# Kernel tuning notes

Measured on AMD Instinct MI355X. Metric: run time of the kernel, lower is better.

## Reference

```python
import jax, jax.numpy as jnp
import numpy as np

TEMPERATURE = 1.0  # anneal_state_params['tempature'] at init
EPS_ZERO = 1e-5
EPS_DIV = 1e-29

N, M, K, D = 200000, 64, 16, 32

def setup_inputs() -> dict:
    key = jax.random.key(0)
    k1, k2, k3 = jax.random.split(key, 3)
    T = jax.random.normal(k1, (N, D), dtype=jnp.float32)
    alpha = jax.random.uniform(k2, (M, K, D), dtype=jnp.float32)  # np.random.rand init
    th = jnp.zeros((M, K), dtype=jnp.float32)
    # ambiguity thresholds: column 0 = pos (>0), column 1 = neg (<0)
    a = jax.random.uniform(k3, (M, K, 2), dtype=jnp.float32) * 0.5 + 0.1
    amb = a * jnp.array([1.0, -1.0], dtype=jnp.float32)
    return {"T": T, "alpha": alpha, "th": th, "amb": amb}

def reference(T, alpha, th, amb):
    # per-fern softmax over the feature axis of alpha*temperature
    sa = jax.nn.softmax(alpha * TEMPERATURE, axis=-1)          # (M, K, D)
    # batched fern projections: one einsum replaces the per-fern matmul loop
    temp = jnp.einsum('nd,mkd->nmk', T, sa)                    # (N, M, K)
    temp = jnp.where(jnp.abs(temp) < EPS_ZERO, 0.0, temp)
    b = temp - th[None, :, :]                                  # subtract threshold
    pos = amb[None, :, :, 0]                                   # (1, M, K)
    neg = amb[None, :, :, 1]
    B = jnp.clip((b - neg) / (pos - neg + EPS_DIV), 0.0, 1.0)  # (N, M, K)
    return B
```

## Files before the change

kernel.cpp:

```cpp
#include <hip/hip_runtime.h>
#include <math.h>

#define N_TOT 200000
#define D_    32
#define MK    1024
#define EPS_ZERO 1e-5f
#define EPS_DIV  1e-29f

#define BN   64
#define BMK  256
#define NB_N (N_TOT / BN)
#define NB_MK (MK / BMK)

typedef __attribute__((ext_vector_type(8))) short short8;
typedef __attribute__((ext_vector_type(4))) float f32x4;

__device__ __forceinline__ unsigned short f2bf(float x) {
    unsigned int u = __float_as_uint(x);
    u += 0x7FFFu + ((u >> 16) & 1u);
    return (unsigned short)(u >> 16);
}
__device__ __forceinline__ float bf2f(unsigned short h) {
    return __uint_as_float(((unsigned int)h) << 16);
}

__global__ __launch_bounds__(256) void prep_kernel(
    const float* __restrict__ alpha, const float* __restrict__ th,
    const float* __restrict__ amb,
    unsigned short* __restrict__ Whi, unsigned short* __restrict__ Wlo,
    float* __restrict__ ot)
{
    int mk = blockIdx.x * 256 + threadIdx.x;
    if (mk >= MK) return;
    float v[D_];
    float mx = -1e30f;
#pragma unroll
    for (int d = 0; d < D_; ++d) { v[d] = alpha[mk * D_ + d]; mx = fmaxf(mx, v[d]); }
    float sum = 0.f;
#pragma unroll
    for (int d = 0; d < D_; ++d) { v[d] = expf(v[d] - mx); sum += v[d]; }
    float pos = amb[mk * 2 + 0];
    float neg = amb[mk * 2 + 1];
    float s  = 1.0f / (pos - neg + EPS_DIV);
    float si = s / sum;
#pragma unroll
    for (int d = 0; d < D_; ++d) {
        float w = v[d] * si;
        unsigned short h = f2bf(w);
        Whi[mk * D_ + d] = h;
        Wlo[mk * D_ + d] = f2bf(w - bf2f(h));
    }
    ot[2 * mk + 0] = (0.0f - th[mk] - neg) * s;
    ot[2 * mk + 1] = EPS_ZERO * s;
}

__global__ __launch_bounds__(256) void fern_mfma(
    const float* __restrict__ T,
    const unsigned short* __restrict__ Whi, const unsigned short* __restrict__ Wlo,
    const float* __restrict__ ot, float* __restrict__ out)
{
    __shared__ __align__(16) short Thi_l[BN][40];
    __shared__ __align__(16) short Tlo_l[BN][40];
    __shared__ __align__(16) short Whi_l[BMK][40];
    __shared__ __align__(16) short Wlo_l[BMK][40];
    __shared__ float2 ot_l[BMK];

    const int tid = threadIdx.x;
    const int bx  = blockIdx.x;
    const int nb  = bx % NB_N;
    const int mkq = bx / NB_N;
    const int n0  = nb * BN;
    const int mk0 = mkq * BMK;

    {
        int row = tid >> 2;
        int d0  = (tid & 3) * 8;
        const float* src = T + (long)(n0 + row) * D_ + d0;
        float4 v0 = *(const float4*)src;
        float4 v1 = *(const float4*)(src + 4);
        float xs[8] = { v0.x, v0.y, v0.z, v0.w, v1.x, v1.y, v1.z, v1.w };
        short8 vh, vl;
#pragma unroll
        for (int j = 0; j < 8; ++j) {
            unsigned short h = f2bf(xs[j]);
            vh[j] = (short)h;
            vl[j] = (short)f2bf(xs[j] - bf2f(h));
        }
        *(short8*)&Thi_l[row][d0] = vh;
        *(short8*)&Tlo_l[row][d0] = vl;
    }
#pragma unroll
    for (int i = 0; i < 4; ++i) {
        int f   = tid + i * 256;
        int col = f >> 2;
        int k0  = (f & 3) * 8;
        *(short8*)&Whi_l[col][k0] = *(const short8*)(Whi + (long)(mk0 + col) * D_ + k0);
        *(short8*)&Wlo_l[col][k0] = *(const short8*)(Wlo + (long)(mk0 + col) * D_ + k0);
    }
    ot_l[tid] = *(const float2*)(ot + 2 * (mk0 + tid));
    __syncthreads();

    const int lane = tid & 63;
    const int wid  = tid >> 6;
    const int lc   = lane & 15;
    const int lk   = lane >> 4;

    short8 ahi = *(const short8*)&Thi_l[wid * 16 + lc][lk * 8];
    short8 alo = *(const short8*)&Tlo_l[wid * 16 + lc][lk * 8];

    long rowbase = ((long)(n0 + wid * 16 + lk * 4)) * MK + mk0 + lc;

#pragma unroll 4
    for (int t = 0; t < 16; ++t) {
        short8 bhi = *(const short8*)&Whi_l[t * 16 + lc][lk * 8];
        short8 blo = *(const short8*)&Wlo_l[t * 16 + lc][lk * 8];
        f32x4 acc = { 0.f, 0.f, 0.f, 0.f };
        acc = __builtin_amdgcn_mfma_f32_16x16x32_bf16(ahi, bhi, acc, 0, 0, 0);
        acc = __builtin_amdgcn_mfma_f32_16x16x32_bf16(alo, bhi, acc, 0, 0, 0);
        acc = __builtin_amdgcn_mfma_f32_16x16x32_bf16(ahi, blo, acc, 0, 0, 0);

        float2 o2 = ot_l[t * 16 + lc];
        float* po = out + rowbase + t * 16;
#pragma unroll
        for (int j = 0; j < 4; ++j) {
            float x = acc[j];
            float y = (fabsf(x) < o2.y) ? o2.x : (x + o2.x);
            po[j * MK] = fminf(fmaxf(y, 0.f), 1.f);
        }
    }
}

extern "C" void kernel_launch(void* const* d_in, const int* in_sizes, int n_in,
                              void* d_out, int out_size, void* d_ws, size_t ws_size,
                              hipStream_t stream)
{
    const float* T     = (const float*)d_in[0];
    const float* alpha = (const float*)d_in[1];
    const float* th    = (const float*)d_in[2];
    const float* amb   = (const float*)d_in[3];
    float* out = (float*)d_out;

    unsigned short* Whi = (unsigned short*)d_ws;
    unsigned short* Wlo = Whi + MK * D_;
    float* ot = (float*)(Wlo + MK * D_);

    prep_kernel<<<MK / 256, 256, 0, stream>>>(alpha, th, amb, Whi, Wlo, ot);
    fern_mfma<<<NB_N * NB_MK, 256, 0, stream>>>(T, Whi, Wlo, ot, out);
}
```

Measured before the change: 201.2 us.

## Use persistent waves holding weight slices in registers, dropping LDS staging

Replaces the one-block-per-tile grid with a fixed grid of 4096 blocks. Each wave owns a 128-column slice of the weights, kept in registers along with the offset/threshold pairs, and loops over 16-row tiles of T. It converts T to hi/lo bf16 directly in registers, with no shared memory and no __syncthreads. This removes the per-block reload of the weights and the LDS round trip, at the cost of higher register pressure (launch bounds of 3 blocks) and more redundant T reads, since eight waves read each T tile.

```diff
diff --git a/kernel.cpp b/kernel.cpp
--- a/kernel.cpp
+++ b/kernel.cpp
@@ -7,10 +7,13 @@
 #define EPS_ZERO 1e-5f
 #define EPS_DIV  1e-29f
 
-#define BN   64
-#define BMK  256
-#define NB_N (N_TOT / BN)
-#define NB_MK (MK / BMK)
+#define ROWS  16
+#define COLS  128
+#define NT    8
+#define NMKE  (MK / COLS)
+#define NTILE (N_TOT / ROWS)
+#define NBLK  4096
+#define WQ    ((NBLK * 4) / NMKE)
 
 typedef __attribute__((ext_vector_type(8))) short short8;
 typedef __attribute__((ext_vector_type(4))) float f32x4;
@@ -54,78 +57,68 @@
     ot[2 * mk + 1] = EPS_ZERO * s;
 }
 
-__global__ __launch_bounds__(256) void fern_mfma(
+__global__ __launch_bounds__(256, 3) void fern_mfma(
     const float* __restrict__ T,
     const unsigned short* __restrict__ Whi, const unsigned short* __restrict__ Wlo,
     const float* __restrict__ ot, float* __restrict__ out)
 {
-    __shared__ __align__(16) short Thi_l[BN][40];
-    __shared__ __align__(16) short Tlo_l[BN][40];
-    __shared__ __align__(16) short Whi_l[BMK][40];
-    __shared__ __align__(16) short Wlo_l[BMK][40];
-    __shared__ float2 ot_l[BMK];
+    const int tid     = threadIdx.x;
+    const int lane    = tid & 63;
+    const int wid     = tid >> 6;
+    const int wave_id = blockIdx.x * 4 + wid;
+    const int mke     = wave_id & (NMKE - 1);
+    const int wq      = wave_id >> 3;
+    const int lc      = lane & 15;
+    const int lk      = lane >> 4;
+    const int mk0     = mke * COLS;
 
-    const int tid = threadIdx.x;
-    const int bx  = blockIdx.x;
-    const int nb  = bx % NB_N;
-    const int mkq = bx / NB_N;
-    const int n0  = nb * BN;
-    const int mk0 = mkq * BMK;
+    short8 wh[NT], wl[NT];
+    float2 o2[NT];
+#pragma unroll
+    for (int t = 0; t < NT; ++t) {
+        long c = (long)(mk0 + t * 16 + lc);
+        wh[t] = *(const short8*)(Whi + c * D_ + lk * 8);
+        wl[t] = *(const short8*)(Wlo + c * D_ + lk * 8);
+        o2[t] = *(const float2*)(ot + 2 * c);
+    }
 
-    {
-        int row = tid >> 2;
-        int d0  = (tid & 3) * 8;
-        const float* src = T + (long)(n0 + row) * D_ + d0;
-        float4 v0 = *(const float4*)src;
-        float4 v1 = *(const float4*)(src + 4);
+    for (int tile = wq; tile < NTILE; tile += WQ) {
+        const int n0 = tile * ROWS;
+
+        const float* tp = T + (long)(n0 + lc) * D_ + lk * 8;
+        float4 v0 = *(const float4*)tp;
+        float4 v1 = *(const float4*)(tp + 4);
         float xs[8] = { v0.x, v0.y, v0.z, v0.w, v1.x, v1.y, v1.z, v1.w };
-        short8 vh, vl;
+        short8 ah, al;
 #pragma unroll
         for (int j = 0; j < 8; ++j) {
             unsigned short h = f2bf(xs[j]);
-            vh[j] = (short)h;
-            vl[j] = (short)f2bf(xs[j] - bf2f(h));
+            ah[j] = (short)h;
+            al[j] = (short)f2bf(xs[j] - bf2f(h));
         }
-        *(short8*)&Thi_l[row][d0] = vh;
-        *(short8*)&Tlo_l[row][d0] = vl;
-    }
+
+        float* r0 = out + ((long)(n0 + lk * 4 + 0)) * MK + mk0 + lc;
+        float* r1 = r0 + MK;
+        float* r2 = r1 + MK;
+        float* r3 = r2 + MK;
+
 #pragma unroll
-    for (int i = 0; i < 4; ++i) {
-        int f   = tid + i * 256;
-        int col = f >> 2;
-        int k0  = (f & 3) * 8;
-        *(short8*)&Whi_l[col][k0] = *(const short8*)(Whi + (long)(mk0 + col) * D_ + k0);
-        *(short8*)&Wlo_l[col][k0] = *(const short8*)(Wlo + (long)(mk0 + col) * D_ + k0);
-    }
-    ot_l[tid] = *(const float2*)(ot + 2 * (mk0 + tid));
-    __syncthreads();
+        for (int t = 0; t < NT; ++t) {
+            f32x4 acc = { 0.f, 0.f, 0.f, 0.f };
+            acc = __builtin_amdgcn_mfma_f32_16x16x32_bf16(ah, wh[t], acc, 0, 0, 0);
+            acc = __builtin_amdgcn_mfma_f32_16x16x32_bf16(al, wh[t], acc, 0, 0, 0);
+            acc = __builtin_amdgcn_mfma_f32_16x16x32_bf16(ah, wl[t], acc, 0, 0, 0);
 
-    const int lane = tid & 63;
-    const int wid  = tid >> 6;
-    const int lc   = lane & 15;
-    const int lk   = lane >> 4;
-
-    short8 ahi = *(const short8*)&Thi_l[wid * 16 + lc][lk * 8];
-    short8 alo = *(const short8*)&Tlo_l[wid * 16 + lc][lk * 8];
-
-    long rowbase = ((long)(n0 + wid * 16 + lk * 4)) * MK + mk0 + lc;
-
-#pragma unroll 4
-    for (int t = 0; t < 16; ++t) {
-        short8 bhi = *(const short8*)&Whi_l[t * 16 + lc][lk * 8];
-        short8 blo = *(const short8*)&Wlo_l[t * 16 + lc][lk * 8];
-        f32x4 acc = { 0.f, 0.f, 0.f, 0.f };
-        acc = __builtin_amdgcn_mfma_f32_16x16x32_bf16(ahi, bhi, acc, 0, 0, 0);
-        acc = __builtin_amdgcn_mfma_f32_16x16x32_bf16(alo, bhi, acc, 0, 0, 0);
-        acc = __builtin_amdgcn_mfma_f32_16x16x32_bf16(ahi, blo, acc, 0, 0, 0);
-
-        float2 o2 = ot_l[t * 16 + lc];
-        float* po = out + rowbase + t * 16;
-#pragma unroll
-        for (int j = 0; j < 4; ++j) {
-            float x = acc[j];
-            float y = (fabsf(x) < o2.y) ? o2.x : (x + o2.x);
-            po[j * MK] = fminf(fmaxf(y, 0.f), 1.f);
+            const float off = o2[t].x, thr = o2[t].y;
+            float x0 = acc[0], x1 = acc[1], x2 = acc[2], x3 = acc[3];
+            x0 = (fabsf(x0) < thr) ? off : (x0 + off);
+            x1 = (fabsf(x1) < thr) ? off : (x1 + off);
+            x2 = (fabsf(x2) < thr) ? off : (x2 + off);
+            x3 = (fabsf(x3) < thr) ? off : (x3 + off);
+            r0[t * 16] = fminf(fmaxf(x0, 0.f), 1.f);
+            r1[t * 16] = fminf(fmaxf(x1, 0.f), 1.f);
+            r2[t * 16] = fminf(fmaxf(x2, 0.f), 1.f);
+            r3[t * 16] = fminf(fmaxf(x3, 0.f), 1.f);
         }
     }
 }
@@ -145,5 +138,5 @@
     float* ot = (float*)(Wlo + MK * D_);
 
     prep_kernel<<<MK / 256, 256, 0, stream>>>(alpha, th, amb, Whi, Wlo, ot);
-    fern_mfma<<<NB_N * NB_MK, 256, 0, stream>>>(T, Whi, Wlo, ot, out);
+    fern_mfma<<<NBLK, 256, 0, stream>>>(T, Whi, Wlo, ot, out);
 }
```

Result: no change. 198.0 us (-1.6%).
